# Kernel tuning notes

Measured on AMD Instinct MI355X. Metric: run time of the kernel, lower is better.

## Reference

```python
import jax, jax.numpy as jnp
import numpy as np

D_MODEL = 512
NHEAD = 4
HEAD_DIM = D_MODEL // NHEAD


def setup_inputs() -> dict:
    key = jax.random.key(0)
    ks = jax.random.split(key, 12)
    B, S = 2, 4096
    s = 1.0 / np.sqrt(D_MODEL)
    inp = {
        "query": jax.random.normal(ks[0], (B, S, D_MODEL), jnp.float32),
        "key": jax.random.normal(ks[1], (B, S, D_MODEL), jnp.float32),
        "value": jax.random.normal(ks[2], (B, S, D_MODEL), jnp.float32),
        "Wq": jax.random.uniform(ks[3], (D_MODEL, D_MODEL), jnp.float32, -s, s),
        "bq": jax.random.uniform(ks[4], (D_MODEL,), jnp.float32, -s, s),
        "Wk": jax.random.uniform(ks[5], (D_MODEL, D_MODEL), jnp.float32, -s, s),
        "bk": jax.random.uniform(ks[6], (D_MODEL,), jnp.float32, -s, s),
        "Wv": jax.random.uniform(ks[7], (D_MODEL, D_MODEL), jnp.float32, -s, s),
        "bv": jax.random.uniform(ks[8], (D_MODEL,), jnp.float32, -s, s),
        "Wo": jax.random.uniform(ks[9], (D_MODEL, D_MODEL), jnp.float32, -s, s),
        "bo": jax.random.uniform(ks[10], (D_MODEL,), jnp.float32, -s, s),
    }
    return inp


def reference(query, key, value, Wq, bq, Wk, bk, Wv, bv, Wo, bo):
    B, Sq, _ = query.shape
    Sk = key.shape[1]
    # projections (torch Linear: x @ W.T + b); split heads -> [B, H, S, hd]
    def proj(x, W, b, S):
        return (x @ W.T + b).reshape(B, S, NHEAD, HEAD_DIM).transpose(0, 2, 1, 3)
    Q = proj(query, Wq, bq, Sq)
    K = proj(key, Wk, bk, Sk)
    V = proj(value, Wv, bv, Sk)
    scale = 1.0 / np.sqrt(HEAD_DIM).astype(np.float32)
    scores = jnp.einsum("bhqd,bhkd->bhqk", Q, K) * scale  # [B,H,Sq,Sk]
    weights = jax.nn.softmax(scores, axis=-1)
    out = jnp.einsum("bhqk,bhkd->bhqd", weights, V)  # [B,H,Sq,hd]
    out = out.transpose(0, 2, 1, 3).reshape(B, Sq, D_MODEL)
    return out @ Wo.T + bo
```

## Files before the change

kernel.cpp:

```cpp
#include <hip/hip_runtime.h>


#define D_MODEL 512
#define NHEAD 4
#define HD 128
#define S_ 4096

typedef __attribute__((ext_vector_type(8))) short bf16x8;
typedef __attribute__((ext_vector_type(4))) short bf16x4;
typedef __attribute__((ext_vector_type(4))) float f32x4;
typedef __attribute__((ext_vector_type(2))) unsigned uint2v;
typedef __attribute__((ext_vector_type(4))) unsigned uint4v;

#define SCQ (0.08838834764831845f * 1.4426950408889634f)

__device__ __forceinline__ short f2bf(float f) {
    unsigned u = __builtin_bit_cast(unsigned, f);
    u += 0x7fffu + ((u >> 16) & 1u);
    return (short)(u >> 16);
}
__device__ __forceinline__ unsigned pk2bf(float a, float b) {
    unsigned ua = __builtin_bit_cast(unsigned, a);
    ua += 0x7fffu + ((ua >> 16) & 1u);
    unsigned ub = __builtin_bit_cast(unsigned, b);
    ub += 0x7fffu + ((ub >> 16) & 1u);
    return (ua >> 16) | (ub & 0xffff0000u);
}
__device__ __forceinline__ void gl2lds16(const short* g, short* l) {
    __builtin_amdgcn_global_load_lds(
        (const __attribute__((address_space(1))) void*)g,
        (__attribute__((address_space(3))) void*)l, 16, 0, 0);
}

__global__ __launch_bounds__(256) void convert_kernel(
    const float* __restrict__ s0, const float* __restrict__ s1,
    const float* __restrict__ s2, const float* __restrict__ s3,
    const float* __restrict__ s4, const float* __restrict__ s5,
    const float* __restrict__ s6,
    short* __restrict__ d0, short* __restrict__ d1, short* __restrict__ d2,
    short* __restrict__ d3, short* __restrict__ d4, short* __restrict__ d5,
    short* __restrict__ d6)
{
    int seg = blockIdx.y;
    const float* src; short* dst; int n;
    const int NBIG = 2 * S_ * D_MODEL;
    const int NW = D_MODEL * D_MODEL;
    switch (seg) {
        case 0: src = s0; dst = d0; n = NBIG; break;
        case 1: src = s1; dst = d1; n = NBIG; break;
        case 2: src = s2; dst = d2; n = NBIG; break;
        case 3: src = s3; dst = d3; n = NW; break;
        case 4: src = s4; dst = d4; n = NW; break;
        case 5: src = s5; dst = d5; n = NW; break;
        default: src = s6; dst = d6; n = NW; break;
    }
    int idx = (blockIdx.x * 256 + threadIdx.x) * 8;
    if (idx >= n) return;
    float4 a = *(const float4*)(src + idx);
    float4 b = *(const float4*)(src + idx + 4);
    uint4v o;
    o[0] = pk2bf(a.x, a.y); o[1] = pk2bf(a.z, a.w);
    o[2] = pk2bf(b.x, b.y); o[3] = pk2bf(b.z, b.w);
    *(uint4v*)(dst + idx) = o;
}

__global__ __launch_bounds__(256) void qkv_kernel(
    const short* __restrict__ qb, const short* __restrict__ kb,
    const short* __restrict__ vb,
    const short* __restrict__ Wqb, const short* __restrict__ Wkb,
    const short* __restrict__ Wvb,
    const float* __restrict__ bq, const float* __restrict__ bk,
    const float* __restrict__ bv,
    short* __restrict__ Qh, short* __restrict__ Kh, short* __restrict__ VT)
{
    __shared__ short smem[12288];
    short* lA = smem;
    short* lB = smem + 4096;
    int z = blockIdx.z;
    const short* A    = (z == 0) ? qb  : (z == 1) ? kb  : vb;
    const short* W    = (z == 0) ? Wqb : (z == 1) ? Wkb : Wvb;
    const float* bias = (z == 0) ? bq  : (z == 1) ? bk  : bv;
    short* out        = (z == 0) ? Qh  : (z == 1) ? Kh  : VT;
    int vmode = (z == 2);
    float osc = (z == 0) ? SCQ : 1.0f;

    int t = threadIdx.x;
    int wv = t >> 6, ln = t & 63, q4 = ln >> 4, c = ln & 15;
    int m0 = blockIdx.x * 64, n0 = blockIdx.y * 128;
    f32x4 acc[8] = {};

    for (int k0 = 0; k0 < 512; k0 += 64) {
        for (int i = 0; i < 2; ++i) {
            int id = i * 256 + t;
            int m = id >> 3, kgp = id & 7;
            gl2lds16(A + (size_t)(m0 + m) * 512 + k0 + ((kgp ^ (m & 7)) << 3),
                     &lA[id * 8]);
        }
        for (int i = 0; i < 4; ++i) {
            int id = i * 256 + t;
            int n = id >> 3, kgp = id & 7;
            gl2lds16(W + (size_t)(n0 + n) * 512 + k0 + ((kgp ^ (n & 7)) << 3),
                     &lB[id * 8]);
        }
        __syncthreads();
        for (int ks = 0; ks < 2; ++ks) {
            int kg = ks * 4 + q4;
            int m = wv * 16 + c;
            bf16x8 af = *(bf16x8*)&lA[m * 64 + ((kg ^ (m & 7)) << 3)];
            bf16x8 bfr[8];
            for (int nt = 0; nt < 8; ++nt) {
                int n = nt * 16 + c;
                bfr[nt] = *(bf16x8*)&lB[n * 64 + ((kg ^ (n & 7)) << 3)];
            }
            for (int nt = 0; nt < 8; ++nt)
                acc[nt] = __builtin_amdgcn_mfma_f32_16x16x32_bf16(af, bfr[nt], acc[nt], 0, 0, 0);
        }
        __syncthreads();
    }

    if (vmode == 0) {
        const int TS = 136;
        short* lT = smem;
        for (int nt = 0; nt < 8; ++nt) {
            float bv_ = bias[n0 + nt * 16 + c];
            for (int r = 0; r < 4; ++r) {
                int srow = wv * 16 + q4 * 4 + r;
                lT[srow * TS + nt * 16 + c] = f2bf((acc[nt][r] + bv_) * osc);
            }
        }
        __syncthreads();
        int bb = m0 >> 12, sbase = m0 & 4095, h = blockIdx.y;
        for (int i = 0; i < 4; ++i) {
            int id = i * 256 + t;
            int row = id >> 4, g = id & 15;
            bf16x8 vv = *(bf16x8*)&lT[row * TS + g * 8];
            *(bf16x8*)&out[((size_t)((bb * NHEAD + h) * S_ + sbase + row)) * HD + g * 8] = vv;
        }
    } else {
        for (int nt = 0; nt < 8; ++nt) {
            int d = nt * 16 + c;
            float bv_ = bias[n0 + d];
            uint2v pv;
            pv[0] = pk2bf(acc[nt][0] + bv_, acc[nt][1] + bv_);
            pv[1] = pk2bf(acc[nt][2] + bv_, acc[nt][3] + bv_);
            int gr = wv * 4 + q4;
            *(uint2v*)&lB[d * 64 + ((gr ^ (d & 15)) << 2)] = pv;
        }
        __syncthreads();
        int bb = m0 >> 12, sbase = m0 & 4095, h = blockIdx.y;
        for (int i = 0; i < 8; ++i) {
            int id = i * 256 + t;
            int d = id >> 4, grl = id & 15;
            bf16x4 v = *(bf16x4*)&lB[d * 64 + ((grl ^ (d & 15)) << 2)];
            *(bf16x4*)&out[((size_t)((bb * NHEAD + h) * HD + d)) * S_ + sbase + grl * 4] = v;
        }
    }
}

__global__ __launch_bounds__(256) void outproj_kernel(
    const short* __restrict__ A, const short* __restrict__ W,
    const float* __restrict__ bias, float* __restrict__ out)
{
    __shared__ short lA[64 * 64];
    __shared__ short lB[128 * 64];
    int t = threadIdx.x;
    int wv = t >> 6, ln = t & 63, q4 = ln >> 4, c = ln & 15;
    int m0 = blockIdx.x * 64, n0 = blockIdx.y * 128;
    f32x4 acc[8] = {};

    for (int k0 = 0; k0 < 512; k0 += 64) {
        for (int i = 0; i < 2; ++i) {
            int id = i * 256 + t;
            int m = id >> 3, kgp = id & 7;
            gl2lds16(A + (size_t)(m0 + m) * 512 + k0 + ((kgp ^ (m & 7)) << 3),
                     &lA[id * 8]);
        }
        for (int i = 0; i < 4; ++i) {
            int id = i * 256 + t;
            int n = id >> 3, kgp = id & 7;
            gl2lds16(W + (size_t)(n0 + n) * 512 + k0 + ((kgp ^ (n & 7)) << 3),
                     &lB[id * 8]);
        }
        __syncthreads();
        for (int ks = 0; ks < 2; ++ks) {
            int kg = ks * 4 + q4;
            int m = wv * 16 + c;
            bf16x8 af = *(bf16x8*)&lA[m * 64 + ((kg ^ (m & 7)) << 3)];
            bf16x8 bfr[8];
            for (int nt = 0; nt < 8; ++nt) {
                int n = nt * 16 + c;
                bfr[nt] = *(bf16x8*)&lB[n * 64 + ((kg ^ (n & 7)) << 3)];
            }
            for (int nt = 0; nt < 8; ++nt)
                acc[nt] = __builtin_amdgcn_mfma_f32_16x16x32_bf16(af, bfr[nt], acc[nt], 0, 0, 0);
        }
        __syncthreads();
    }

    for (int nt = 0; nt < 8; ++nt) {
        int col = n0 + nt * 16 + c;
        float bv_ = bias[col];
        for (int r = 0; r < 4; ++r) {
            int mrow = m0 + wv * 16 + q4 * 4 + r;
            out[(size_t)mrow * 512 + col] = acc[nt][r] + bv_;
        }
    }
}

__global__ __launch_bounds__(256, 2) void flash_kernel(
    const short* __restrict__ Qh, const short* __restrict__ Kh,
    const short* __restrict__ VTg, short* __restrict__ AO,
    float* __restrict__ U, float* __restrict__ ML, int nsplit, int kkspan)
{
    __shared__ short lK[64 * 128];
    __shared__ short lVT[128 * 64];
    __shared__ short lP[128 * 64];
    __shared__ float lL[2][128];
    int t = threadIdx.x;
    int wv = t >> 6, ln = t & 63, q4 = ln >> 4, c = ln & 15;
    int wi = wv >> 1, wj = wv & 1;
    int bh = blockIdx.x;
    int s0 = blockIdx.y * 128;
    int z = blockIdx.z;
    const size_t base = (size_t)bh * S_ * HD;

    bf16x8 qf[4][4];
    for (int qt = 0; qt < 4; ++qt) {
        int s = s0 + wi * 64 + qt * 16 + c;
        const short* qp = Qh + base + (size_t)s * HD + q4 * 8;
        for (int ks = 0; ks < 4; ++ks)
            qf[qt][ks] = *(const bf16x8*)(qp + ks * 32);
    }

    f32x4 of[4][4] = {};
    float lrun[4] = {};

    int kkbeg = z * kkspan, kkend = kkbeg + kkspan;
    for (int kk0 = kkbeg; kk0 < kkend; kk0 += 64) {
        for (int i = 0; i < 4; ++i) {
            int id = i * 256 + t;
            int m = id >> 4, kgp = id & 15;
            gl2lds16(Kh + base + (size_t)(kk0 + m) * HD + ((kgp ^ (m & 7)) << 3),
                     &lK[id * 8]);
            int mv = id >> 3, kgvp = id & 7;
            gl2lds16(VTg + base + (size_t)mv * S_ + kk0 + ((kgvp ^ (mv & 7)) << 3),
                     &lVT[id * 8]);
        }
        __syncthreads();

        f32x4 sf[4][2] = {};
        for (int ks = 0; ks < 4; ++ks) {
            int kg = ks * 4 + q4;
            bf16x8 af[2];
            for (int kt = 0; kt < 2; ++kt) {
                int row = wj * 32 + kt * 16 + c;
                af[kt] = *(bf16x8*)&lK[row * 128 + ((kg ^ (row & 7)) << 3)];
            }
            for (int qt = 0; qt < 4; ++qt)
                for (int kt = 0; kt < 2; ++kt)
                    sf[qt][kt] = __builtin_amdgcn_mfma_f32_16x16x32_bf16(
                        af[kt], qf[qt][ks], sf[qt][kt], 0, 0, 0);
        }

        for (int qt = 0; qt < 4; ++qt) {
            float lt = 0.f;
            int row = wi * 64 + qt * 16 + c;
            for (int kt = 0; kt < 2; ++kt) {
                float p0 = exp2f(sf[qt][kt][0]);
                float p1 = exp2f(sf[qt][kt][1]);
                float p2 = exp2f(sf[qt][kt][2]);
                float p3 = exp2f(sf[qt][kt][3]);
                lt += (p0 + p1) + (p2 + p3);
                uint2v pv;
                pv[0] = pk2bf(p0, p1);
                pv[1] = pk2bf(p2, p3);
                int g = wj * 4 + kt * 2 + (q4 >> 1);
                *(uint2v*)&lP[row * 64 + ((g ^ (row & 7)) << 3) + ((q4 & 1) << 2)] = pv;
            }
            lt += __shfl_xor(lt, 16);
            lt += __shfl_xor(lt, 32);
            if (q4 == 0) lL[wj][wi * 64 + qt * 16 + c] = lt;
        }
        __syncthreads();

        for (int qt = 0; qt < 4; ++qt) {
            int q = wi * 64 + qt * 16 + c;
            lrun[qt] += lL[0][q] + lL[1][q];
        }

        for (int ksv = 0; ksv < 2; ++ksv) {
            int kg = ksv * 4 + q4;
            bf16x8 av[4], bp[4];
            for (int dt = 0; dt < 4; ++dt) {
                int row = wj * 64 + dt * 16 + c;
                av[dt] = *(bf16x8*)&lVT[row * 64 + ((kg ^ (row & 7)) << 3)];
            }
            for (int qt = 0; qt < 4; ++qt) {
                int row = wi * 64 + qt * 16 + c;
                bp[qt] = *(bf16x8*)&lP[row * 64 + ((kg ^ (row & 7)) << 3)];
            }
            for (int qt = 0; qt < 4; ++qt)
                for (int dt = 0; dt < 4; ++dt)
                    of[dt][qt] = __builtin_amdgcn_mfma_f32_16x16x32_bf16(
                        av[dt], bp[qt], of[dt][qt], 0, 0, 0);
        }
        __syncthreads();
    }

    if (nsplit > 1) {
        for (int qt = 0; qt < 4; ++qt) {
            int s = s0 + wi * 64 + qt * 16 + c;
            size_t rowu = (size_t)(z * 8 + bh) * S_ + s;
            float* up = U + rowu * HD;
            for (int dt = 0; dt < 4; ++dt)
                *(f32x4*)&up[wj * 64 + dt * 16 + q4 * 4] = of[dt][qt];
            if (q4 == 0 && wj == 0) ML[rowu] = lrun[qt];
        }
    } else {
        int b = bh >> 2, h = bh & 3;
        for (int qt = 0; qt < 4; ++qt) {
            float inv = 1.0f / lrun[qt];
            int s = s0 + wi * 64 + qt * 16 + c;
            short* dst = AO + ((size_t)(b * S_ + s)) * D_MODEL + h * HD;
            for (int dt = 0; dt < 4; ++dt) {
                uint2v ov;
                ov[0] = pk2bf(of[dt][qt][0] * inv, of[dt][qt][1] * inv);
                ov[1] = pk2bf(of[dt][qt][2] * inv, of[dt][qt][3] * inv);
                *(uint2v*)(dst + wj * 64 + dt * 16 + q4 * 4) = ov;
            }
        }
    }
}

__global__ __launch_bounds__(256) void combine_kernel(
    const float* __restrict__ U, const float* __restrict__ ML,
    short* __restrict__ AO, int nsplit)
{
    int row = blockIdx.x * 8 + (threadIdx.x >> 5);
    int d4 = (threadIdx.x & 31) * 4;
    const int R = 8 * S_;
    float l = 0.f;
    f32x4 u = {0.f, 0.f, 0.f, 0.f};
    for (int zz = 0; zz < nsplit; ++zz) {
        l += ML[(size_t)zz * R + row];
        f32x4 uz = *(const f32x4*)&U[((size_t)zz * R + row) * HD + d4];
        u += uz;
    }
    float inv = 1.0f / l;
    uint2v o;
    o[0] = pk2bf(u[0] * inv, u[1] * inv);
    o[1] = pk2bf(u[2] * inv, u[3] * inv);
    int bh = row >> 12, s = row & 4095;
    int b = bh >> 2, h = bh & 3;
    *(uint2v*)&AO[((size_t)(b * S_ + s)) * D_MODEL + h * HD + d4] = o;
}

extern "C" void kernel_launch(void* const* d_in, const int* in_sizes, int n_in,
                              void* d_out, int out_size, void* d_ws, size_t ws_size,
                              hipStream_t stream) {
    const float* q  = (const float*)d_in[0];
    const float* k  = (const float*)d_in[1];
    const float* v  = (const float*)d_in[2];
    const float* Wq = (const float*)d_in[3];
    const float* bq = (const float*)d_in[4];
    const float* Wk = (const float*)d_in[5];
    const float* bk = (const float*)d_in[6];
    const float* Wv = (const float*)d_in[7];
    const float* bv = (const float*)d_in[8];
    const float* Wo = (const float*)d_in[9];
    const float* bo = (const float*)d_in[10];

    const size_t HS = (size_t)2 * NHEAD * S_ * HD;
    const size_t NBIG = HS;
    const size_t NW = (size_t)D_MODEL * D_MODEL;
    const size_t R = (size_t)8 * S_;

    char* wsb = (char*)d_ws;
    short* Qh = (short*)wsb;
    short* Kh = Qh + HS;
    short* VT = Kh + HS;
    short* AO = VT + HS;
    char* r2 = wsb + 4 * HS * 2;
    short* qb  = (short*)r2;
    short* kb  = qb + NBIG;
    short* vb  = kb + NBIG;
    short* Wqb = vb + NBIG;
    short* Wkb = Wqb + NW;
    short* Wvb = Wkb + NW;
    float* U   = (float*)r2;

    int nsplit = 1;
    size_t r2sz = 3 * NBIG * 2 + 3 * NW * 2;
    for (int cand = 4; cand >= 2; cand -= 2) {
        size_t r2c = (size_t)cand * R * HD * 4;
        if (r2c < 3 * NBIG * 2 + 3 * NW * 2) r2c = 3 * NBIG * 2 + 3 * NW * 2;
        size_t need = 4 * HS * 2 + r2c + (size_t)cand * R * 4 + NW * 2;
        if (ws_size >= need) { nsplit = cand; r2sz = r2c; break; }
    }
    float* ML  = (float*)(r2 + r2sz);
    short* Wob = (short*)((char*)ML + (size_t)nsplit * R * 4);
    int kkspan = S_ / nsplit;

    dim3 blk(256);
    convert_kernel<<<dim3(2048, 7), blk, 0, stream>>>(
        q, k, v, Wq, Wk, Wv, Wo, qb, kb, vb, Wqb, Wkb, Wvb, Wob);
    qkv_kernel<<<dim3(128, 4, 3), blk, 0, stream>>>(
        qb, kb, vb, Wqb, Wkb, Wvb, bq, bk, bv, Qh, Kh, VT);
    flash_kernel<<<dim3(8, 32, nsplit), blk, 0, stream>>>(
        Qh, Kh, VT, AO, U, ML, nsplit, kkspan);
    if (nsplit > 1)
        combine_kernel<<<dim3(S_), blk, 0, stream>>>(U, ML, AO, nsplit);
    outproj_kernel<<<dim3(128, 4), blk, 0, stream>>>(AO, Wob, bo, (float*)d_out);
}
```

Measured before the change: 255.0 us.

## Double-buffer K tiles and give each wave full rows in flash kernel

The flash attention kernel gets a double-buffered K tile in LDS and prefetches the next K (and, after the PV step, the next V^T) tile with async global-to-LDS loads. Hand-placed vmcnt waits and raw barriers replace the __syncthreads calls. Work is repartitioned so each wave owns 32 query rows across all keys and head dims, which removes the cross-wave row-sum exchange through LDS and one barrier per iteration. MFMA sections are wrapped in s_setprio. In exchange, LDS use grows by 16 KB and each wave holds more accumulator registers, which may lower occupancy. The vmcnt counts are hand-tuned and could break correctness if the load counts change.

After: 249.0 us. 2.3% less time.

```diff
diff --git a/kernel.cpp b/kernel.cpp
--- a/kernel.cpp
+++ b/kernel.cpp
@@ -212,60 +212,91 @@
     const short* __restrict__ VTg, short* __restrict__ AO,
     float* __restrict__ U, float* __restrict__ ML, int nsplit, int kkspan)
 {
-    __shared__ short lK[64 * 128];
+    __shared__ short lK[2][64 * 128];
     __shared__ short lVT[128 * 64];
     __shared__ short lP[128 * 64];
-    __shared__ float lL[2][128];
     int t = threadIdx.x;
     int wv = t >> 6, ln = t & 63, q4 = ln >> 4, c = ln & 15;
-    int wi = wv >> 1, wj = wv & 1;
     int bh = blockIdx.x;
     int s0 = blockIdx.y * 128;
     int z = blockIdx.z;
     const size_t base = (size_t)bh * S_ * HD;
 
-    bf16x8 qf[4][4];
-    for (int qt = 0; qt < 4; ++qt) {
-        int s = s0 + wi * 64 + qt * 16 + c;
+    bf16x8 qf[2][4];
+    #pragma unroll
+    for (int qt = 0; qt < 2; ++qt) {
+        int s = s0 + wv * 32 + qt * 16 + c;
         const short* qp = Qh + base + (size_t)s * HD + q4 * 8;
+        #pragma unroll
         for (int ks = 0; ks < 4; ++ks)
             qf[qt][ks] = *(const bf16x8*)(qp + ks * 32);
     }
 
-    f32x4 of[4][4] = {};
-    float lrun[4] = {};
-
-    int kkbeg = z * kkspan, kkend = kkbeg + kkspan;
-    for (int kk0 = kkbeg; kk0 < kkend; kk0 += 64) {
-        for (int i = 0; i < 4; ++i) {
-            int id = i * 256 + t;
-            int m = id >> 4, kgp = id & 15;
-            gl2lds16(Kh + base + (size_t)(kk0 + m) * HD + ((kgp ^ (m & 7)) << 3),
-                     &lK[id * 8]);
-            int mv = id >> 3, kgvp = id & 7;
-            gl2lds16(VTg + base + (size_t)mv * S_ + kk0 + ((kgvp ^ (mv & 7)) << 3),
-                     &lVT[id * 8]);
-        }
-        __syncthreads();
-
-        f32x4 sf[4][2] = {};
+    f32x4 of[8][2] = {};
+    float lrun[2] = {};
+
+    int kkbeg = z * kkspan;
+    int nt = kkspan >> 6;
+
+    #pragma unroll
+    for (int i = 0; i < 4; ++i) {
+        int id = i * 256 + t;
+        int m = id >> 4, kgp = id & 15;
+        gl2lds16(Kh + base + (size_t)(kkbeg + m) * HD + ((kgp ^ (m & 7)) << 3),
+                 &lK[0][id * 8]);
+    }
+    #pragma unroll
+    for (int i = 0; i < 4; ++i) {
+        int id = i * 256 + t;
+        int mv = id >> 3, kgvp = id & 7;
+        gl2lds16(VTg + base + (size_t)mv * S_ + kkbeg + ((kgvp ^ (mv & 7)) << 3),
+                 &lVT[id * 8]);
+    }
+    asm volatile("s_waitcnt vmcnt(4)" ::: "memory");
+    __builtin_amdgcn_s_barrier();
+    __builtin_amdgcn_sched_barrier(0);
+
+    int cur = 0;
+    for (int it = 0; it < nt; ++it) {
+        int kk0 = kkbeg + it * 64;
+        int more = (it + 1 < nt);
+
+        if (more) {
+            #pragma unroll
+            for (int i = 0; i < 4; ++i) {
+                int id = i * 256 + t;
+                int m = id >> 4, kgp = id & 15;
+                gl2lds16(Kh + base + (size_t)(kk0 + 64 + m) * HD + ((kgp ^ (m & 7)) << 3),
+                         &lK[cur ^ 1][id * 8]);
+            }
+        }
+
+        f32x4 sf[2][4] = {};
+        __builtin_amdgcn_s_setprio(1);
+        #pragma unroll
         for (int ks = 0; ks < 4; ++ks) {
             int kg = ks * 4 + q4;
-            bf16x8 af[2];
-            for (int kt = 0; kt < 2; ++kt) {
-                int row = wj * 32 + kt * 16 + c;
-                af[kt] = *(bf16x8*)&lK[row * 128 + ((kg ^ (row & 7)) << 3)];
-            }
-            for (int qt = 0; qt < 4; ++qt)
-                for (int kt = 0; kt < 2; ++kt)
+            bf16x8 af[4];
+            #pragma unroll
+            for (int kt = 0; kt < 4; ++kt) {
+                int row = kt * 16 + c;
+                af[kt] = *(bf16x8*)&lK[cur][row * 128 + ((kg ^ (row & 7)) << 3)];
+            }
+            #pragma unroll
+            for (int qt = 0; qt < 2; ++qt)
+                #pragma unroll
+                for (int kt = 0; kt < 4; ++kt)
                     sf[qt][kt] = __builtin_amdgcn_mfma_f32_16x16x32_bf16(
                         af[kt], qf[qt][ks], sf[qt][kt], 0, 0, 0);
         }
-
-        for (int qt = 0; qt < 4; ++qt) {
+        __builtin_amdgcn_s_setprio(0);
+
+        #pragma unroll
+        for (int qt = 0; qt < 2; ++qt) {
             float lt = 0.f;
-            int row = wi * 64 + qt * 16 + c;
-            for (int kt = 0; kt < 2; ++kt) {
+            int row = wv * 32 + qt * 16 + c;
+            #pragma unroll
+            for (int kt = 0; kt < 4; ++kt) {
                 float p0 = exp2f(sf[qt][kt][0]);
                 float p1 = exp2f(sf[qt][kt][1]);
                 float p2 = exp2f(sf[qt][kt][2]);
@@ -274,59 +305,83 @@
                 uint2v pv;
                 pv[0] = pk2bf(p0, p1);
                 pv[1] = pk2bf(p2, p3);
-                int g = wj * 4 + kt * 2 + (q4 >> 1);
+                int g = kt * 2 + (q4 >> 1);
                 *(uint2v*)&lP[row * 64 + ((g ^ (row & 7)) << 3) + ((q4 & 1) << 2)] = pv;
             }
             lt += __shfl_xor(lt, 16);
             lt += __shfl_xor(lt, 32);
-            if (q4 == 0) lL[wj][wi * 64 + qt * 16 + c] = lt;
-        }
-        __syncthreads();
-
-        for (int qt = 0; qt < 4; ++qt) {
-            int q = wi * 64 + qt * 16 + c;
-            lrun[qt] += lL[0][q] + lL[1][q];
-        }
-
+            lrun[qt] += lt;
+        }
+
+        if (more) asm volatile("s_waitcnt vmcnt(4)" ::: "memory");
+        else      asm volatile("s_waitcnt vmcnt(0)" ::: "memory");
+        __builtin_amdgcn_s_barrier();
+        __builtin_amdgcn_sched_barrier(0);
+
+        __builtin_amdgcn_s_setprio(1);
+        #pragma unroll
         for (int ksv = 0; ksv < 2; ++ksv) {
             int kg = ksv * 4 + q4;
-            bf16x8 av[4], bp[4];
-            for (int dt = 0; dt < 4; ++dt) {
-                int row = wj * 64 + dt * 16 + c;
+            bf16x8 av[8], bp[2];
+            #pragma unroll
+            for (int dt = 0; dt < 8; ++dt) {
+                int row = dt * 16 + c;
                 av[dt] = *(bf16x8*)&lVT[row * 64 + ((kg ^ (row & 7)) << 3)];
             }
-            for (int qt = 0; qt < 4; ++qt) {
-                int row = wi * 64 + qt * 16 + c;
+            #pragma unroll
+            for (int qt = 0; qt < 2; ++qt) {
+                int row = wv * 32 + qt * 16 + c;
                 bp[qt] = *(bf16x8*)&lP[row * 64 + ((kg ^ (row & 7)) << 3)];
             }
-            for (int qt = 0; qt < 4; ++qt)
-                for (int dt = 0; dt < 4; ++dt)
+            #pragma unroll
+            for (int qt = 0; qt < 2; ++qt)
+                #pragma unroll
+                for (int dt = 0; dt < 8; ++dt)
                     of[dt][qt] = __builtin_amdgcn_mfma_f32_16x16x32_bf16(
                         av[dt], bp[qt], of[dt][qt], 0, 0, 0);
         }
-        __syncthreads();
+        __builtin_amdgcn_s_setprio(0);
+
+        asm volatile("s_waitcnt vmcnt(0)" ::: "memory");
+        __builtin_amdgcn_s_barrier();
+        __builtin_amdgcn_sched_barrier(0);
+
+        if (more) {
+            #pragma unroll
+            for (int i = 0; i < 4; ++i) {
+                int id = i * 256 + t;
+                int mv = id >> 3, kgvp = id & 7;
+                gl2lds16(VTg + base + (size_t)mv * S_ + kk0 + 64 + ((kgvp ^ (mv & 7)) << 3),
+                         &lVT[id * 8]);
+            }
+        }
+        cur ^= 1;
     }
 
     if (nsplit > 1) {
-        for (int qt = 0; qt < 4; ++qt) {
-            int s = s0 + wi * 64 + qt * 16 + c;
+        #pragma unroll
+        for (int qt = 0; qt < 2; ++qt) {
+            int s = s0 + wv * 32 + qt * 16 + c;
             size_t rowu = (size_t)(z * 8 + bh) * S_ + s;
             float* up = U + rowu * HD;
-            for (int dt = 0; dt < 4; ++dt)
-                *(f32x4*)&up[wj * 64 + dt * 16 + q4 * 4] = of[dt][qt];
-            if (q4 == 0 && wj == 0) ML[rowu] = lrun[qt];
+            #pragma unroll
+            for (int dt = 0; dt < 8; ++dt)
+                *(f32x4*)&up[dt * 16 + q4 * 4] = of[dt][qt];
+            if (q4 == 0) ML[rowu] = lrun[qt];
         }
     } else {
         int b = bh >> 2, h = bh & 3;
-        for (int qt = 0; qt < 4; ++qt) {
+        #pragma unroll
+        for (int qt = 0; qt < 2; ++qt) {
             float inv = 1.0f / lrun[qt];
-            int s = s0 + wi * 64 + qt * 16 + c;
+            int s = s0 + wv * 32 + qt * 16 + c;
             short* dst = AO + ((size_t)(b * S_ + s)) * D_MODEL + h * HD;
-            for (int dt = 0; dt < 4; ++dt) {
+            #pragma unroll
+            for (int dt = 0; dt < 8; ++dt) {
                 uint2v ov;
                 ov[0] = pk2bf(of[dt][qt][0] * inv, of[dt][qt][1] * inv);
                 ov[1] = pk2bf(of[dt][qt][2] * inv, of[dt][qt][3] * inv);
-                *(uint2v*)(dst + wj * 64 + dt * 16 + q4 * 4) = ov;
+                *(uint2v*)(dst + dt * 16 + q4 * 4) = ov;
             }
         }
     }
```
